# Kernel tuning notes

Measured on AMD Instinct MI355X. Metric: run time of the kernel, lower is better.

Reference implementation:

```python
import jax, jax.numpy as jnp
import numpy as np

DIM = 1024
NH = 16
HD = DIM // NH  # 64
NT = max(1, int(NH * 0.25))  # 4 time heads
NS = NH - NT                 # 12 space heads
SCALE = HD ** (-0.5)


def setup_inputs() -> dict:
    key = jax.random.key(0)
    ks = jax.random.split(key, 8)
    B, T = 2, 2048
    init = 0.02
    return {
        "x": jax.random.normal(ks[0], (B, T, DIM), dtype=jnp.float32),
        # weights stored as (in, out); torch Linear y = x @ W.T is equivalent
        "Wqt": jax.random.normal(ks[1], (DIM, NT * HD), dtype=jnp.float32) * init,
        "Wkt": jax.random.normal(ks[2], (DIM, NT * HD), dtype=jnp.float32) * init,
        "Wqs": jax.random.normal(ks[3], (DIM, NS * HD), dtype=jnp.float32) * init,
        "Wks": jax.random.normal(ks[4], (DIM, NS * HD), dtype=jnp.float32) * init,
        "Wv": jax.random.normal(ks[5], (DIM, DIM), dtype=jnp.float32) * init,
        "Wout": jax.random.normal(ks[6], (DIM, DIM), dtype=jnp.float32) * init,
        "bout": jnp.zeros((DIM,), dtype=jnp.float32),
        "w_sigma": jnp.zeros((1,), dtype=jnp.float32),
    }


def reference(x, Wqt, Wkt, Wqs, Wks, Wv, Wout, bout, w_sigma):
    B, T, D = x.shape
    Qt = (x @ Wqt).reshape(B, T, NT, HD)
    Kt = (x @ Wkt).reshape(B, T, NT, HD)
    Qs = (x @ Wqs).reshape(B, T, NS, HD)
    Ks = (x @ Wks).reshape(B, T, NS, HD)
    st = jnp.einsum('bthd,bshd->bths', Qt, Kt)  # [B,T,NT,T]
    ss = jnp.einsum('bthd,bshd->bths', Qs, Ks)  # [B,T,NS,T]
    sig = jax.nn.sigmoid(w_sigma)  # shape (1,), broadcasts
    score = jnp.concatenate([-sig * st, ss], axis=2) * SCALE  # [B,T,NH,T]
    attn = jax.nn.softmax(score, axis=-1)
    V = (x @ Wv).reshape(B, T, NH, HD)
    ctx = jnp.einsum('bths,bshd->bthd', attn, V).reshape(B, T, D)
    return ctx @ Wout + bout
```

## Files before the change

### kernel.cpp

```cpp
#include <hip/hip_runtime.h>
#include <hip/hip_bf16.h>

typedef __bf16 bf16_t;
typedef __bf16 bf16x4 __attribute__((ext_vector_type(4)));
typedef __bf16 bf16x8 __attribute__((ext_vector_type(8)));
typedef float  f32x4  __attribute__((ext_vector_type(4)));

#define DIM     1024
#define NHEAD   16
#define HDIM    64
#define NTIME   4
#define TSEQ    2048
#define NBATCH  2
#define SCALE_F 0.125f
#define LOG2E   1.4426950408889634f

#define GLL(gp, lp) __builtin_amdgcn_global_load_lds( \
    (const __attribute__((address_space(1))) unsigned int*)(const void*)(gp), \
    (__attribute__((address_space(3))) unsigned int*)(void*)(lp), 16, 0, 0)

#define OFF_WQKVT 0UL
#define OFF_WOUTT (OFF_WQKVT + 3072UL*1024UL*2UL)
#define OFF_Q     (OFF_WOUTT + 1024UL*1024UL*2UL)
#define OFF_K     (OFF_Q  + 2UL*16UL*2048UL*64UL*2UL)
#define OFF_VT    (OFF_K  + 2UL*16UL*2048UL*64UL*2UL)
#define OFF_CTX   (OFF_VT + 2UL*16UL*2048UL*64UL*2UL)

__global__ void prep_all(const float* __restrict__ x,
                         const float* __restrict__ Wqt, const float* __restrict__ Wkt,
                         const float* __restrict__ Wqs, const float* __restrict__ Wks,
                         const float* __restrict__ Wv,  const float* __restrict__ Wout,
                         bf16_t* __restrict__ Xb, bf16_t* __restrict__ WqkvT,
                         bf16_t* __restrict__ WoutT) {
    __shared__ float T[64][65];
    const int bid = blockIdx.x;
    if (bid < 2048) {
        int i = bid * 256 + threadIdx.x;
        const float4* s = (const float4*)(x + (size_t)i * 8);
        float4 a = s[0], b2 = s[1];
        bf16x8 v;
        v[0] = (bf16_t)a.x;  v[1] = (bf16_t)a.y;  v[2] = (bf16_t)a.z;  v[3] = (bf16_t)a.w;
        v[4] = (bf16_t)b2.x; v[5] = (bf16_t)b2.y; v[6] = (bf16_t)b2.z; v[7] = (bf16_t)b2.w;
        *(bf16x8*)(Xb + (size_t)i * 8) = v;
        return;
    }
    const int tc = threadIdx.x & 63, tr = threadIdx.x >> 6;
    if (bid < 2816) {
        const int l = bid - 2048;
        const int n0 = (l % 48) * 64;
        const int k0 = (l / 48) * 64;
        const int region = n0 >> 10;
        const int cc = n0 & 1023;
        const int h = cc >> 6;
        const float* src; int ncols, col0;
        if (region == 2) { src = Wv; ncols = 1024; col0 = cc; }
        else if (h < NTIME) { src = (region == 0) ? Wqt : Wkt; ncols = NTIME * HDIM; col0 = h * HDIM; }
        else                { src = (region == 0) ? Wqs : Wks; ncols = (NHEAD - NTIME) * HDIM; col0 = (h - NTIME) * HDIM; }
#pragma unroll
        for (int i = 0; i < 16; ++i) {
            int kl = tr * 16 + i;
            T[kl][tc] = src[(size_t)(k0 + kl) * ncols + col0 + tc];
        }
        __syncthreads();
#pragma unroll
        for (int i = 0; i < 16; ++i) {
            int nl = tr * 16 + i;
            WqkvT[(size_t)(n0 + nl) * 1024 + k0 + tc] = (bf16_t)T[tc][nl];
        }
    } else {
        const int l = bid - 2816;
        const int n0 = (l % 16) * 64;
        const int k0 = (l / 16) * 64;
#pragma unroll
        for (int i = 0; i < 16; ++i) {
            int kl = tr * 16 + i;
            T[kl][tc] = Wout[(size_t)(k0 + kl) * 1024 + n0 + tc];
        }
        __syncthreads();
#pragma unroll
        for (int i = 0; i < 16; ++i) {
            int nl = tr * 16 + i;
            WoutT[(size_t)(n0 + nl) * 1024 + k0 + tc] = (bf16_t)T[tc][nl];
        }
    }
}

template<int MODE, int NB>
__global__ __launch_bounds__(256)
void gemm_bf16(const bf16_t* __restrict__ Ab, const bf16_t* __restrict__ Bt,
               bf16_t* __restrict__ Qb, bf16_t* __restrict__ Kb, bf16_t* __restrict__ Vt,
               float* __restrict__ Cout, const float* __restrict__ bias)
{
    __shared__ __align__(16) bf16_t As[128][64];
    __shared__ __align__(16) bf16_t Bs[128][64];

    const int cpx = gridDim.x >> 3;
    const int l = (blockIdx.x & 7) * cpx + (blockIdx.x >> 3);
    const int m0 = (l / NB) * 128, n0 = (l % NB) * 128;

    const int tid  = threadIdx.x;
    const int lane = tid & 63;
    const int wave = tid >> 6;
    const int wm = (wave >> 1) * 64, wn = (wave & 1) * 64;
    const int g = lane >> 4, lr = lane & 15;

    f32x4 acc[4][4];
#pragma unroll
    for (int i = 0; i < 4; ++i)
#pragma unroll
        for (int j = 0; j < 4; ++j) acc[i][j] = f32x4{0.f, 0.f, 0.f, 0.f};

    for (int k0 = 0; k0 < 1024; k0 += 64) {
        __syncthreads();
#pragma unroll
        for (int c = 0; c < 4; ++c) {
            int idx  = tid + c * 256;
            int row  = idx >> 3;
            int csrc = (idx & 7) ^ (row & 7);
            GLL(Ab + (size_t)(m0 + row) * 1024 + k0 + csrc * 8,
                (char*)&As[0][0] + (c * 256 + wave * 64) * 16);
            GLL(Bt + (size_t)(n0 + row) * 1024 + k0 + csrc * 8,
                (char*)&Bs[0][0] + (c * 256 + wave * 64) * 16);
        }
        __syncthreads();

#pragma unroll
        for (int kk = 0; kk < 2; ++kk) {
            bf16x8 afr[4], bfr[4];
#pragma unroll
            for (int f = 0; f < 4; ++f) {
                int ra = wm + f * 16 + lr;
                afr[f] = *(const bf16x8*)((const char*)&As[0][0] + ra * 128 + (((kk * 4 + g) ^ (ra & 7)) << 4));
                int rb = wn + f * 16 + lr;
                bfr[f] = *(const bf16x8*)((const char*)&Bs[0][0] + rb * 128 + (((kk * 4 + g) ^ (rb & 7)) << 4));
            }
#pragma unroll
            for (int fm = 0; fm < 4; ++fm)
#pragma unroll
                for (int fn = 0; fn < 4; ++fn)
                    acc[fm][fn] = __builtin_amdgcn_mfma_f32_16x16x32_bf16(bfr[fn], afr[fm], acc[fm][fn], 0, 0, 0);
        }
    }

    const int region = n0 >> 10;
#pragma unroll
    for (int fm = 0; fm < 4; ++fm) {
        const int m = m0 + wm + fm * 16 + lr;
        const int b = m >> 11, t = m & 2047;
#pragma unroll
        for (int fn = 0; fn < 4; ++fn) {
            const int nb = n0 + wn + fn * 16 + g * 4;
            if constexpr (MODE == 1) {
                float4 bb = *(const float4*)(bias + nb);
                float4 v;
                v.x = acc[fm][fn][0] + bb.x;
                v.y = acc[fm][fn][1] + bb.y;
                v.z = acc[fm][fn][2] + bb.z;
                v.w = acc[fm][fn][3] + bb.w;
                *(float4*)(Cout + (size_t)m * DIM + nb) = v;
            } else {
                const int cc = nb & 1023;
                const int h = cc >> 6, d0 = cc & 63;
                const size_t bh = (size_t)(b * NHEAD + h);
                if (region == 2) {
#pragma unroll
                    for (int r = 0; r < 4; ++r)
                        Vt[(bh * HDIM + d0 + r) * TSEQ + t] = (bf16_t)acc[fm][fn][r];
                } else {
                    bf16x4 w;
#pragma unroll
                    for (int r = 0; r < 4; ++r) w[r] = (bf16_t)acc[fm][fn][r];
                    bf16_t* dst = (region == 0) ? Qb : Kb;
                    *(bf16x4*)(dst + (bh * TSEQ + t) * HDIM + d0) = w;
                }
            }
        }
    }
}

__global__ __launch_bounds__(256, 3)
void attn_kernel(const bf16_t* __restrict__ Qb, const bf16_t* __restrict__ Kb,
                 const bf16_t* __restrict__ Vt, bf16_t* __restrict__ ctx,
                 const float* __restrict__ w_sigma)
{
    __shared__ __align__(16) bf16_t Ktile[2][64][64];
    __shared__ __align__(16) bf16_t Vtile[2][64][64];
    __shared__ __align__(16) char   P2[4][4096];

    const int l    = ((blockIdx.x & 7) << 6) + (blockIdx.x >> 3);
    const int qc   = l & 15;
    const int bh   = l >> 4;
    const int h    = bh & 15;
    const int b    = bh >> 4;
    const int tid  = threadIdx.x;
    const int lane = tid & 63;
    const int wave = tid >> 6;
    const int g = lane >> 4, lr = lane & 15;
    const int q0 = qc * 128 + wave * 32;

    const float sig = 1.f / (1.f + __expf(-w_sigma[0]));
    const float fl2 = ((h < NTIME) ? (-sig * SCALE_F) : SCALE_F) * LOG2E;

    const bf16_t* Qp = Qb + (size_t)bh * TSEQ * HDIM;
    const bf16_t* Kp = Kb + (size_t)bh * TSEQ * HDIM;
    const bf16_t* Vp = Vt + (size_t)bh * HDIM * TSEQ;

    bf16x8 qa0 = *(const bf16x8*)(Qp + (size_t)(q0 + lr) * HDIM + g * 8);
    bf16x8 qa1 = *(const bf16x8*)(Qp + (size_t)(q0 + lr) * HDIM + 32 + g * 8);
    bf16x8 qb0 = *(const bf16x8*)(Qp + (size_t)(q0 + 16 + lr) * HDIM + g * 8);
    bf16x8 qb1 = *(const bf16x8*)(Qp + (size_t)(q0 + 16 + lr) * HDIM + 32 + g * 8);
#pragma unroll
    for (int e = 0; e < 8; ++e) {
        qa0[e] = (bf16_t)((float)qa0[e] * fl2);
        qa1[e] = (bf16_t)((float)qa1[e] * fl2);
        qb0[e] = (bf16_t)((float)qb0[e] * fl2);
        qb1[e] = (bf16_t)((float)qb1[e] * fl2);
    }

    f32x4 oA[4], oB[4];
#pragma unroll
    for (int n = 0; n < 4; ++n) { oA[n] = f32x4{0.f,0.f,0.f,0.f}; oB[n] = f32x4{0.f,0.f,0.f,0.f}; }
    float lpA = 0.f, lpB = 0.f;

    char* const P2w = &P2[wave][0];
    const int qsw = (lr & 7) << 4;

    const int trow = tid >> 3;
    const int tcg  = tid & 7;

    auto stage = [&](int s0, int buf) {
#pragma unroll
        for (int j = 0; j < 2; ++j) {
            int kr = j * 32 + trow;
            GLL(Kp + (size_t)(s0 + kr) * HDIM + ((tcg ^ (kr & 7)) << 3),
                (char*)&Ktile[buf][0][0] + (j * 256 + wave * 64) * 16);
            int vr = j * 32 + trow;
            GLL(Vp + (size_t)vr * TSEQ + s0 + ((tcg ^ (vr & 7)) << 3),
                (char*)&Vtile[buf][0][0] + (j * 256 + wave * 64) * 16);
        }
    };

    auto compute = [&](const char* Kt, const char* Vc) {
        __builtin_amdgcn_s_setprio(1);
#pragma unroll
        for (int st = 0; st < 4; ++st) {
            const int srow = st * 16 + lr;
            const int rs7 = lr & 7;
            bf16x8 kb0 = *(const bf16x8*)(Kt + srow * 128 + ((g ^ rs7) << 4));
            bf16x8 kb1 = *(const bf16x8*)(Kt + srow * 128 + (((4 + g) ^ rs7) << 4));
            f32x4 zA = f32x4{0.f,0.f,0.f,0.f}, zB = f32x4{0.f,0.f,0.f,0.f};
            zA = __builtin_amdgcn_mfma_f32_16x16x32_bf16(kb0, qa0, zA, 0, 0, 0);
            zA = __builtin_amdgcn_mfma_f32_16x16x32_bf16(kb1, qa1, zA, 0, 0, 0);
            zB = __builtin_amdgcn_mfma_f32_16x16x32_bf16(kb0, qb0, zB, 0, 0, 0);
            zB = __builtin_amdgcn_mfma_f32_16x16x32_bf16(kb1, qb1, zB, 0, 0, 0);
            float a0 = __builtin_amdgcn_exp2f(zA[0]);
            float a1 = __builtin_amdgcn_exp2f(zA[1]);
            float a2 = __builtin_amdgcn_exp2f(zA[2]);
            float a3 = __builtin_amdgcn_exp2f(zA[3]);
            float b0 = __builtin_amdgcn_exp2f(zB[0]);
            float b1 = __builtin_amdgcn_exp2f(zB[1]);
            float b2 = __builtin_amdgcn_exp2f(zB[2]);
            float b3 = __builtin_amdgcn_exp2f(zB[3]);
            bf16x4 wA, wB;
            wA[0] = (bf16_t)a0; wA[1] = (bf16_t)a1; wA[2] = (bf16_t)a2; wA[3] = (bf16_t)a3;
            wB[0] = (bf16_t)b0; wB[1] = (bf16_t)b1; wB[2] = (bf16_t)b2; wB[3] = (bf16_t)b3;
            *(bf16x4*)(P2w +        lr * 128 + ((st * 32 + g * 8) ^ qsw)) = wA;
            *(bf16x4*)(P2w + 2048 + lr * 128 + ((st * 32 + g * 8) ^ qsw)) = wB;
            lpA += (a0 + a1) + (a2 + a3);
            lpB += (b0 + b1) + (b2 + b3);
        }
        __builtin_amdgcn_s_setprio(0);

        asm volatile("s_waitcnt lgkmcnt(0)" ::: "memory");
        __builtin_amdgcn_sched_barrier(0);

        __builtin_amdgcn_s_setprio(1);
#pragma unroll
        for (int kc = 0; kc < 2; ++kc) {
            bf16x8 paA = *(const bf16x8*)(P2w +        lr * 128 + ((kc * 64 + g * 16) ^ qsw));
            bf16x8 paB = *(const bf16x8*)(P2w + 2048 + lr * 128 + ((kc * 64 + g * 16) ^ qsw));
#pragma unroll
            for (int n = 0; n < 4; ++n) {
                const int row = n * 16 + lr;
                bf16x8 vb = *(const bf16x8*)(Vc + row * 128 + (((kc * 4 + g) ^ (row & 7)) << 4));
                oA[n] = __builtin_amdgcn_mfma_f32_16x16x32_bf16(vb, paA, oA[n], 0, 0, 0);
                oB[n] = __builtin_amdgcn_mfma_f32_16x16x32_bf16(vb, paB, oB[n], 0, 0, 0);
            }
        }
        __builtin_amdgcn_s_setprio(0);
    };

    const char* const K0 = (const char*)&Ktile[0][0][0];
    const char* const K1 = (const char*)&Ktile[1][0][0];
    const char* const V0 = (const char*)&Vtile[0][0][0];
    const char* const V1 = (const char*)&Vtile[1][0][0];

    stage(0, 0);
    __syncthreads();

#pragma unroll 2
    for (int step = 0; step < 32; ++step) {
        const int cur = step & 1;
        if (step < 31) stage((step + 1) * 64, cur ^ 1);
        compute(cur ? K1 : K0, cur ? V1 : V0);
        __syncthreads();
    }

    float lfA = lpA, lfB = lpB;
    lfA += __shfl_xor(lfA, 16, 64);
    lfA += __shfl_xor(lfA, 32, 64);
    lfB += __shfl_xor(lfB, 16, 64);
    lfB += __shfl_xor(lfB, 32, 64);
    float liA = 1.f / lfA, liB = 1.f / lfB;

    const int tA = q0 + lr, tB = q0 + 16 + lr;
#pragma unroll
    for (int n = 0; n < 4; ++n) {
        bf16x4 wA, wB;
#pragma unroll
        for (int r = 0; r < 4; ++r) {
            wA[r] = (bf16_t)(oA[n][r] * liA);
            wB[r] = (bf16_t)(oB[n][r] * liB);
        }
        *(bf16x4*)(ctx + ((size_t)(b * TSEQ + tA)) * DIM + h * HDIM + n * 16 + g * 4) = wA;
        *(bf16x4*)(ctx + ((size_t)(b * TSEQ + tB)) * DIM + h * HDIM + n * 16 + g * 4) = wB;
    }
}

extern "C" void kernel_launch(void* const* d_in, const int* in_sizes, int n_in,
                              void* d_out, int out_size, void* d_ws, size_t ws_size,
                              hipStream_t stream) {
    const float* x    = (const float*)d_in[0];
    const float* Wqt  = (const float*)d_in[1];
    const float* Wkt  = (const float*)d_in[2];
    const float* Wqs  = (const float*)d_in[3];
    const float* Wks  = (const float*)d_in[4];
    const float* Wv   = (const float*)d_in[5];
    const float* Wout = (const float*)d_in[6];
    const float* bout = (const float*)d_in[7];
    const float* wsig = (const float*)d_in[8];
    (void)in_sizes; (void)n_in; (void)out_size; (void)ws_size;

    char* ws = (char*)d_ws;
    bf16_t* WqkvT = (bf16_t*)(ws + OFF_WQKVT);
    bf16_t* WoutT = (bf16_t*)(ws + OFF_WOUTT);
    bf16_t* Qb    = (bf16_t*)(ws + OFF_Q);
    bf16_t* Kb    = (bf16_t*)(ws + OFF_K);
    bf16_t* Vt    = (bf16_t*)(ws + OFF_VT);
    bf16_t* ctx   = (bf16_t*)(ws + OFF_CTX);
    bf16_t* Xb    = ctx;
    float*  out   = (float*)d_out;

    prep_all<<<3072, 256, 0, stream>>>(x, Wqt, Wkt, Wqs, Wks, Wv, Wout, Xb, WqkvT, WoutT);

    gemm_bf16<0, 24><<<768, 256, 0, stream>>>(Xb, WqkvT, Qb, Kb, Vt, nullptr, nullptr);

    attn_kernel<<<512, 256, 0, stream>>>(Qb, Kb, Vt, ctx, wsig);

    gemm_bf16<1, 8><<<256, 256, 0, stream>>>(ctx, WoutT, nullptr, nullptr, nullptr, out, bout);
}
```

Before: 121.4 us.

## Load attention K tiles straight into registers instead of staging through LDS

The K tile is no longer copied into shared memory. Each lane loads its K fragments directly from global memory into double-buffered registers (kA/kB), and the next tile's loads are issued between the QK MFMAs and the exp stage to hide latency. Only V is still staged in LDS. This cuts LDS traffic and footprint, but raises register pressure, so launch bounds drop from 3 to 2 blocks per CU. The risk is lower occupancy and uncoalesced, L2-dependent K reads, with every wave in a block fetching the same K rows separately.

```diff
diff --git a/kernel.cpp b/kernel.cpp
--- a/kernel.cpp
+++ b/kernel.cpp
@@ -178,12 +178,11 @@
     }
 }
 
-__global__ __launch_bounds__(256, 3)
+__global__ __launch_bounds__(256, 2)
 void attn_kernel(const bf16_t* __restrict__ Qb, const bf16_t* __restrict__ Kb,
                  const bf16_t* __restrict__ Vt, bf16_t* __restrict__ ctx,
                  const float* __restrict__ w_sigma)
 {
-    __shared__ __align__(16) bf16_t Ktile[2][64][64];
     __shared__ __align__(16) bf16_t Vtile[2][64][64];
     __shared__ __align__(16) char   P2[4][4096];
 
@@ -228,39 +227,60 @@
     const int trow = tid >> 3;
     const int tcg  = tid & 7;
 
-    auto stage = [&](int s0, int buf) {
+    auto stageV = [&](int s0, int buf) {
 #pragma unroll
         for (int j = 0; j < 2; ++j) {
-            int kr = j * 32 + trow;
-            GLL(Kp + (size_t)(s0 + kr) * HDIM + ((tcg ^ (kr & 7)) << 3),
-                (char*)&Ktile[buf][0][0] + (j * 256 + wave * 64) * 16);
             int vr = j * 32 + trow;
             GLL(Vp + (size_t)vr * TSEQ + s0 + ((tcg ^ (vr & 7)) << 3),
                 (char*)&Vtile[buf][0][0] + (j * 256 + wave * 64) * 16);
         }
     };
 
-    auto compute = [&](const char* Kt, const char* Vc) {
+    bf16x8 kA[4][2], kB[4][2];
+
+    auto kloadA = [&](int s0) {
+#pragma unroll
+        for (int st = 0; st < 4; ++st) {
+            const bf16_t* p = Kp + (size_t)(s0 + st * 16 + lr) * HDIM + g * 8;
+            kA[st][0] = *(const bf16x8*)p;
+            kA[st][1] = *(const bf16x8*)(p + 32);
+        }
+    };
+    auto kloadB = [&](int s0) {
+#pragma unroll
+        for (int st = 0; st < 4; ++st) {
+            const bf16_t* p = Kp + (size_t)(s0 + st * 16 + lr) * HDIM + g * 8;
+            kB[st][0] = *(const bf16x8*)p;
+            kB[st][1] = *(const bf16x8*)(p + 32);
+        }
+    };
+
+    auto compute = [&](bf16x8 (&kreg)[4][2], const char* Vc, int s0_next, bool loadA) {
+        f32x4 zA[4], zB[4];
         __builtin_amdgcn_s_setprio(1);
 #pragma unroll
         for (int st = 0; st < 4; ++st) {
-            const int srow = st * 16 + lr;
-            const int rs7 = lr & 7;
-            bf16x8 kb0 = *(const bf16x8*)(Kt + srow * 128 + ((g ^ rs7) << 4));
-            bf16x8 kb1 = *(const bf16x8*)(Kt + srow * 128 + (((4 + g) ^ rs7) << 4));
-            f32x4 zA = f32x4{0.f,0.f,0.f,0.f}, zB = f32x4{0.f,0.f,0.f,0.f};
-            zA = __builtin_amdgcn_mfma_f32_16x16x32_bf16(kb0, qa0, zA, 0, 0, 0);
-            zA = __builtin_amdgcn_mfma_f32_16x16x32_bf16(kb1, qa1, zA, 0, 0, 0);
-            zB = __builtin_amdgcn_mfma_f32_16x16x32_bf16(kb0, qb0, zB, 0, 0, 0);
-            zB = __builtin_amdgcn_mfma_f32_16x16x32_bf16(kb1, qb1, zB, 0, 0, 0);
-            float a0 = __builtin_amdgcn_exp2f(zA[0]);
-            float a1 = __builtin_amdgcn_exp2f(zA[1]);
-            float a2 = __builtin_amdgcn_exp2f(zA[2]);
-            float a3 = __builtin_amdgcn_exp2f(zA[3]);
-            float b0 = __builtin_amdgcn_exp2f(zB[0]);
-            float b1 = __builtin_amdgcn_exp2f(zB[1]);
-            float b2 = __builtin_amdgcn_exp2f(zB[2]);
-            float b3 = __builtin_amdgcn_exp2f(zB[3]);
+            f32x4 za = f32x4{0.f,0.f,0.f,0.f}, zb = f32x4{0.f,0.f,0.f,0.f};
+            za = __builtin_amdgcn_mfma_f32_16x16x32_bf16(kreg[st][0], qa0, za, 0, 0, 0);
+            za = __builtin_amdgcn_mfma_f32_16x16x32_bf16(kreg[st][1], qa1, za, 0, 0, 0);
+            zb = __builtin_amdgcn_mfma_f32_16x16x32_bf16(kreg[st][0], qb0, zb, 0, 0, 0);
+            zb = __builtin_amdgcn_mfma_f32_16x16x32_bf16(kreg[st][1], qb1, zb, 0, 0, 0);
+            zA[st] = za; zB[st] = zb;
+        }
+        __builtin_amdgcn_s_setprio(0);
+
+        if (s0_next < TSEQ) { if (loadA) kloadA(s0_next); else kloadB(s0_next); }
+
+#pragma unroll
+        for (int st = 0; st < 4; ++st) {
+            float a0 = __builtin_amdgcn_exp2f(zA[st][0]);
+            float a1 = __builtin_amdgcn_exp2f(zA[st][1]);
+            float a2 = __builtin_amdgcn_exp2f(zA[st][2]);
+            float a3 = __builtin_amdgcn_exp2f(zA[st][3]);
+            float b0 = __builtin_amdgcn_exp2f(zB[st][0]);
+            float b1 = __builtin_amdgcn_exp2f(zB[st][1]);
+            float b2 = __builtin_amdgcn_exp2f(zB[st][2]);
+            float b3 = __builtin_amdgcn_exp2f(zB[st][3]);
             bf16x4 wA, wB;
             wA[0] = (bf16_t)a0; wA[1] = (bf16_t)a1; wA[2] = (bf16_t)a2; wA[3] = (bf16_t)a3;
             wB[0] = (bf16_t)b0; wB[1] = (bf16_t)b1; wB[2] = (bf16_t)b2; wB[3] = (bf16_t)b3;
@@ -269,7 +289,6 @@
             lpA += (a0 + a1) + (a2 + a3);
             lpB += (b0 + b1) + (b2 + b3);
         }
-        __builtin_amdgcn_s_setprio(0);
 
         asm volatile("s_waitcnt lgkmcnt(0)" ::: "memory");
         __builtin_amdgcn_sched_barrier(0);
@@ -290,19 +309,22 @@
         __builtin_amdgcn_s_setprio(0);
     };
 
-    const char* const K0 = (const char*)&Ktile[0][0][0];
-    const char* const K1 = (const char*)&Ktile[1][0][0];
     const char* const V0 = (const char*)&Vtile[0][0][0];
     const char* const V1 = (const char*)&Vtile[1][0][0];
 
-    stage(0, 0);
+    stageV(0, 0);
+    kloadA(0);
     __syncthreads();
 
-#pragma unroll 2
-    for (int step = 0; step < 32; ++step) {
-        const int cur = step & 1;
-        if (step < 31) stage((step + 1) * 64, cur ^ 1);
-        compute(cur ? K1 : K0, cur ? V1 : V0);
+    for (int it = 0; it < 16; ++it) {
+        const int sA = it * 128;
+        if (sA + 64 < TSEQ) stageV(sA + 64, 1);
+        compute(kA, V0, sA + 64, false);
+        __syncthreads();
+
+        const int sB = sA + 64;
+        if (sB + 64 < TSEQ) stageV(sB + 64, 0);
+        compute(kB, V1, sB + 64, true);
         __syncthreads();
     }
 
```

Result: slower. 143.3 us (+18.0%).
